# Kernel optimization log

Measured on AMD Instinct MI355X. Metric: run time of the kernel, lower is better.

Reference implementation:

```python
import jax, jax.numpy as jnp
import numpy as np

D_MODEL = 768
D_STATE = 16
D_CONV = 4
EXPAND = 2
HEADDIM = 64
D_INNER = EXPAND * D_MODEL          # 1536
NHEADS = D_INNER // HEADDIM         # 24
CONV_DIM = D_INNER + 2 * D_STATE    # 1568
D_IN_PROJ = 2 * D_INNER + 2 * D_STATE + NHEADS  # 3128
BATCH, SEQ = 4, 2048


def _mamba_params(key, scale=0.02):
    ks = jax.random.split(key, 5)
    return dict(
        in_w=jax.random.normal(ks[0], (D_MODEL, D_IN_PROJ), jnp.float32) * scale,
        conv_w=jax.random.normal(ks[1], (CONV_DIM, D_CONV), jnp.float32) * scale,
        conv_b=jnp.zeros((CONV_DIM,), jnp.float32),
        dt_bias=jax.random.normal(ks[2], (NHEADS,), jnp.float32) * 0.1,
        A_log=jnp.log(jax.random.uniform(ks[3], (NHEADS,), jnp.float32, 1.0, 16.0)),
        D=jnp.ones((NHEADS,), jnp.float32),
        norm_w=jnp.ones((D_INNER,), jnp.float32),
        out_w=jax.random.normal(ks[4], (D_INNER, D_MODEL), jnp.float32) * scale,
    )


def setup_inputs() -> dict:
    key = jax.random.key(0)
    kx, kf, kb, k1, k2 = jax.random.split(key, 5)
    f = _mamba_params(kf)
    b = _mamba_params(kb)
    k1a, k1b = jax.random.split(k1)
    inp = {
        'x': jax.random.normal(kx, (BATCH, SEQ, D_MODEL), jnp.float32),
        'ln1_w': jnp.ones((D_MODEL,), jnp.float32), 'ln1_b': jnp.zeros((D_MODEL,), jnp.float32),
        'ln2_w': jnp.ones((D_MODEL,), jnp.float32), 'ln2_b': jnp.zeros((D_MODEL,), jnp.float32),
        'ffn_w1': jax.random.normal(k1a, (2 * D_MODEL, 4 * D_MODEL), jnp.float32) * 0.02,
        'ffn_b1': jnp.zeros((4 * D_MODEL,), jnp.float32),
        'ffn_w2': jax.random.normal(k1b, (4 * D_MODEL, D_MODEL), jnp.float32) * 0.02,
        'ffn_b2': jnp.zeros((D_MODEL,), jnp.float32),
    }
    for name, p in (('f', f), ('b', b)):
        for k, v in p.items():
            inp[name + '_' + k] = v
    return inp


def _layernorm(x, w, b, eps=1e-5):
    m = jnp.mean(x, -1, keepdims=True)
    v = jnp.mean((x - m) ** 2, -1, keepdims=True)
    return (x - m) * jax.lax.rsqrt(v + eps) * w + b


def _mamba2(u, in_w, conv_w, conv_b, dt_bias, A_log, D, norm_w, out_w):
    b, l, _ = u.shape
    zxbcdt = u @ in_w                               # (b,l,d_in_proj)
    z = zxbcdt[..., :D_INNER]
    xBC = zxbcdt[..., D_INNER:D_INNER + CONV_DIM]
    dt = jax.nn.softplus(zxbcdt[..., -NHEADS:] + dt_bias)   # (b,l,h)
    # depthwise causal conv1d (kernel D_CONV) + SiLU
    xpad = jnp.pad(xBC, ((0, 0), (D_CONV - 1, 0), (0, 0)))
    xc = sum(conv_w[:, k] * xpad[:, k:k + l, :] for k in range(D_CONV)) + conv_b
    xc = jax.nn.silu(xc)
    xh = xc[..., :D_INNER].reshape(b, l, NHEADS, HEADDIM)
    Bm = xc[..., D_INNER:D_INNER + D_STATE]          # (b,l,n), ngroups=1
    Cm = xc[..., D_INNER + D_STATE:]                 # (b,l,n)
    A = -jnp.exp(A_log)                              # (h,)
    dA = jnp.exp(dt * A)                             # (b,l,h)

    def step(h, inp):
        dA_t, dt_t, B_t, C_t, x_t = inp              # (b,h),(b,h),(b,n),(b,n),(b,h,p)
        h = h * dA_t[:, :, None, None] + (dt_t[:, :, None] * x_t)[..., None] * B_t[:, None, None, :]
        y = jnp.einsum('bhpn,bn->bhp', h, C_t)
        return h, y

    h0 = jnp.zeros((b, NHEADS, HEADDIM, D_STATE), u.dtype)
    xs = (dA.transpose(1, 0, 2), dt.transpose(1, 0, 2), Bm.transpose(1, 0, 2),
          Cm.transpose(1, 0, 2), xh.transpose(1, 0, 2, 3))
    _, ys = jax.lax.scan(step, h0, xs)               # ys: (l,b,h,p)
    y = ys.transpose(1, 0, 2, 3) + D[None, None, :, None] * xh
    y = y.reshape(b, l, D_INNER)
    # gated RMSNorm: rmsnorm(y * silu(z)) * weight
    yz = y * jax.nn.silu(z)
    yz = yz * jax.lax.rsqrt(jnp.mean(yz * yz, -1, keepdims=True) + 1e-5) * norm_w
    return yz @ out_w


def reference(x, ln1_w, ln1_b, ln2_w, ln2_b,
              f_in_w, f_conv_w, f_conv_b, f_dt_bias, f_A_log, f_D, f_norm_w, f_out_w,
              b_in_w, b_conv_w, b_conv_b, b_dt_bias, b_A_log, b_D, b_norm_w, b_out_w,
              ffn_w1, ffn_b1, ffn_w2, ffn_b2):
    xn = _layernorm(x, ln1_w, ln1_b)
    fo = _mamba2(xn, f_in_w, f_conv_w, f_conv_b, f_dt_bias, f_A_log, f_D, f_norm_w, f_out_w)
    bo = _mamba2(jnp.flip(xn, 1), b_in_w, b_conv_w, b_conv_b, b_dt_bias, b_A_log, b_D, b_norm_w, b_out_w)
    bo = jnp.flip(bo, 1)
    bi = jnp.concatenate([fo, bo], -1)
    h = jax.nn.gelu(bi @ ffn_w1 + ffn_b1, approximate=False)
    h = jax.nn.gelu(h @ ffn_w2 + ffn_b2, approximate=False)
    # dropout is identity in eval mode
    return _layernorm(x + h, ln2_w, ln2_b)
```

## Files before the change

### kernel.cpp

```cpp
#include <hip/hip_runtime.h>
#include <math.h>

#define BATCH   4
#define SEQ     2048
#define DMODEL  768
#define DSTATE  16
#define DCONV   4
#define HEADDIM 64
#define DINNER  1536
#define NHEADS  24
#define CONVDIM 1568
#define DINPROJ 3128
#define DFFN    3072
#define ROWS    (BATCH*SEQ)
#define QCH     128
#define NCHUNK  (SEQ/QCH)

typedef __attribute__((ext_vector_type(8))) short bhalf8;
typedef __attribute__((ext_vector_type(4))) float floatx4;

__device__ __forceinline__ float gelu_f(float x) {
    return 0.5f * x * (1.0f + erff(x * 0.70710678118654752f));
}

__device__ __forceinline__ void splitT(float v, unsigned short& h, unsigned short& l) {
    unsigned u = __float_as_uint(v);
    h = (unsigned short)(u >> 16);
    float rem = v - __uint_as_float(u & 0xFFFF0000u);
    l = (unsigned short)(__float_as_uint(rem) >> 16);
}

__device__ __forceinline__ float2 blockReduce2(float a, float b) {
    #pragma unroll
    for (int o = 32; o > 0; o >>= 1) {
        a += __shfl_down(a, o, 64);
        b += __shfl_down(b, o, 64);
    }
    __shared__ float sa[4], sb[4];
    int w = threadIdx.x >> 6, lane = threadIdx.x & 63;
    if (lane == 0) { sa[w] = a; sb[w] = b; }
    __syncthreads();
    if (threadIdx.x == 0) {
        int nw = blockDim.x >> 6;
        for (int i = 1; i < nw; ++i) { a += sa[i]; b += sb[i]; }
        sa[0] = a; sb[0] = b;
    }
    __syncthreads();
    return make_float2(sa[0], sb[0]);
}

__global__ __launch_bounds__(256) void ln_kernel(
    const float* __restrict__ x, const float* __restrict__ res,
    const float* __restrict__ w, const float* __restrict__ b,
    float* __restrict__ out)
{
    int r = blockIdx.x;
    const float* xr = x + (size_t)r * DMODEL;
    float v[3]; float s = 0.f, ss = 0.f;
    #pragma unroll
    for (int i = 0; i < 3; ++i) {
        int c = threadIdx.x + i * 256;
        float t = xr[c];
        if (res) t += res[(size_t)r * DMODEL + c];
        v[i] = t; s += t; ss += t * t;
    }
    float2 red = blockReduce2(s, ss);
    float mean = red.x * (1.0f / DMODEL);
    float var  = red.y * (1.0f / DMODEL) - mean * mean;
    float inv  = rsqrtf(var + 1e-5f);
    #pragma unroll
    for (int i = 0; i < 3; ++i) {
        int c = threadIdx.x + i * 256;
        out[(size_t)r * DMODEL + c] = (v[i] - mean) * inv * w[c] + b[c];
    }
}

__global__ __launch_bounds__(256) void wconv(
    const float* __restrict__ W, unsigned short* __restrict__ TH,
    unsigned short* __restrict__ TL, int K, int N)
{
    __shared__ float t[32][33];
    int tx = threadIdx.x & 31, ty = threadIdx.x >> 5;
    int kb = blockIdx.y * 32, nb = blockIdx.x * 32;
    #pragma unroll
    for (int i = 0; i < 4; ++i) {
        int k = kb + ty + i * 8, n = nb + tx;
        t[ty + i * 8][tx] = (k < K && n < N) ? W[(size_t)k * N + n] : 0.f;
    }
    __syncthreads();
    #pragma unroll
    for (int i = 0; i < 4; ++i) {
        int n = nb + ty + i * 8, k = kb + tx;
        if (n < N && k < K) {
            float v = t[tx][ty + i * 8];
            unsigned u = __float_as_uint(v);
            unsigned rr = u + 0x7FFFu + ((u >> 16) & 1u);
            unsigned short hi = (unsigned short)(rr >> 16);
            float rem = v - __uint_as_float(((unsigned)hi) << 16);
            unsigned u2 = __float_as_uint(rem);
            unsigned r2 = u2 + 0x7FFFu + ((u2 >> 16) & 1u);
            unsigned short lo = (unsigned short)(r2 >> 16);
            TH[(size_t)n * K + k] = hi;
            TL[(size_t)n * K + k] = lo;
        }
    }
}

__global__ __launch_bounds__(256) void gemm3(
    const float* __restrict__ Ag,
    const unsigned short* __restrict__ BHg, const unsigned short* __restrict__ BLg,
    float* __restrict__ C, const float* __restrict__ bias,
    int M, int N, int K, int lda, int ldc, int coloff,
    int revA, int revC, int act)
{
    __shared__ unsigned short AsH[128 * 40], AsL[128 * 40];
    __shared__ unsigned short BsH[128 * 40], BsL[128 * 40];

    const int tid = threadIdx.x;
    const int m0 = blockIdx.y * 128;
    const int n0 = blockIdx.x * 128;

    const int r  = tid >> 1;
    const int sg = (tid & 1) * 16;
    int arow = m0 + r;
    if (revA) arow = (arow & ~(SEQ - 1)) + (SEQ - 1 - (arow & (SEQ - 1)));
    const size_t abase = (size_t)arow * lda;
    const int brow = n0 + r;
    const bool bok = brow < N;
    const size_t bbase = (size_t)brow * K;

    float4 fa[4];
    bhalf8 rb0, rb1, rb2, rb3;
    const bhalf8 bz = {0, 0, 0, 0, 0, 0, 0, 0};

    auto gload = [&](int k0) {
        size_t ao = abase + k0 + sg;
        #pragma unroll
        for (int q = 0; q < 4; ++q) fa[q] = *(const float4*)(Ag + ao + 4 * q);
        if (bok) {
            size_t bo = bbase + k0 + sg;
            rb0 = *(const bhalf8*)(BHg + bo);
            rb1 = *(const bhalf8*)(BHg + bo + 8);
            rb2 = *(const bhalf8*)(BLg + bo);
            rb3 = *(const bhalf8*)(BLg + bo + 8);
        } else { rb0 = bz; rb1 = bz; rb2 = bz; rb3 = bz; }
    };

    auto stage = [&]() {
        const float* fs = (const float*)fa;
        bhalf8 h0, h1, l0, l1;
        #pragma unroll
        for (int e = 0; e < 8; ++e) {
            unsigned short h, l;
            splitT(fs[e], h, l);     h0[e] = (short)h; l0[e] = (short)l;
            splitT(fs[8 + e], h, l); h1[e] = (short)h; l1[e] = (short)l;
        }
        *(bhalf8*)&AsH[r * 40 + sg]     = h0;
        *(bhalf8*)&AsH[r * 40 + sg + 8] = h1;
        *(bhalf8*)&AsL[r * 40 + sg]     = l0;
        *(bhalf8*)&AsL[r * 40 + sg + 8] = l1;
        *(bhalf8*)&BsH[r * 40 + sg]     = rb0;
        *(bhalf8*)&BsH[r * 40 + sg + 8] = rb1;
        *(bhalf8*)&BsL[r * 40 + sg]     = rb2;
        *(bhalf8*)&BsL[r * 40 + sg + 8] = rb3;
    };

    const int w = tid >> 6, lane = tid & 63;
    const int rw = (w >> 1) * 64, cw = (w & 1) * 64;
    const int lr = lane & 15;
    const int lq = lane >> 4;

    floatx4 acc[4][4];
    const floatx4 fz = {0.f, 0.f, 0.f, 0.f};
    #pragma unroll
    for (int i = 0; i < 4; ++i)
        #pragma unroll
        for (int j = 0; j < 4; ++j) acc[i][j] = fz;

    const int ktiles = K >> 5;
    gload(0);
    for (int kt = 0; kt < ktiles; ++kt) {
        __syncthreads();
        stage();
        __syncthreads();
        if (kt + 1 < ktiles) gload((kt + 1) * 32);

        bhalf8 ah[4], al[4], bh[4], bl[4];
        #pragma unroll
        for (int i = 0; i < 4; ++i) {
            ah[i] = *(const bhalf8*)&AsH[(rw + i * 16 + lr) * 40 + lq * 8];
            al[i] = *(const bhalf8*)&AsL[(rw + i * 16 + lr) * 40 + lq * 8];
            bh[i] = *(const bhalf8*)&BsH[(cw + i * 16 + lr) * 40 + lq * 8];
            bl[i] = *(const bhalf8*)&BsL[(cw + i * 16 + lr) * 40 + lq * 8];
        }
        #pragma unroll
        for (int i = 0; i < 4; ++i)
            #pragma unroll
            for (int j = 0; j < 4; ++j) {
                acc[i][j] = __builtin_amdgcn_mfma_f32_16x16x32_bf16(ah[i], bh[j], acc[i][j], 0, 0, 0);
                acc[i][j] = __builtin_amdgcn_mfma_f32_16x16x32_bf16(ah[i], bl[j], acc[i][j], 0, 0, 0);
                acc[i][j] = __builtin_amdgcn_mfma_f32_16x16x32_bf16(al[i], bh[j], acc[i][j], 0, 0, 0);
            }
    }

    #pragma unroll
    for (int i = 0; i < 4; ++i) {
        #pragma unroll
        for (int j = 0; j < 4; ++j) {
            int gc = n0 + cw + j * 16 + lr;
            if (gc < N) {
                float bv = bias ? bias[gc] : 0.f;
                #pragma unroll
                for (int rg = 0; rg < 4; ++rg) {
                    int gm = m0 + rw + i * 16 + lq * 4 + rg;
                    if (revC) gm = (gm & ~(SEQ - 1)) + (SEQ - 1 - (gm & (SEQ - 1)));
                    float v = acc[i][j][rg] + bv;
                    if (act) v = gelu_f(v);
                    C[(size_t)gm * ldc + coloff + gc] = v;
                }
            }
        }
    }
}

__global__ __launch_bounds__(256) void conv_kernel(
    const float* __restrict__ zx, const float* __restrict__ cw,
    const float* __restrict__ cb, float* __restrict__ xcv,
    float* __restrict__ bc)
{
    int c = blockIdx.x * 256 + threadIdx.x;
    int r = blockIdx.y;
    if (c >= CONVDIM) return;
    int t = r & (SEQ - 1);
    int rb = r & ~(SEQ - 1);
    float acc = cb[c];
    #pragma unroll
    for (int k = 0; k < DCONV; ++k) {
        int tt = t - (DCONV - 1) + k;
        if (tt >= 0)
            acc += cw[c * DCONV + k] * zx[(size_t)(rb + tt) * DINPROJ + DINNER + c];
    }
    float v = acc / (1.0f + expf(-acc));
    if (c < DINNER) xcv[(size_t)r * DINNER + c] = v;
    else            bc[(size_t)r * 32 + (c - DINNER)] = v;
}

__global__ __launch_bounds__(256) void dt_kernel(
    const float* __restrict__ zx, const float* __restrict__ dt_bias,
    const float* __restrict__ A_log, float* __restrict__ dtda)
{
    int i = blockIdx.x * 256 + threadIdx.x;
    if (i >= ROWS * NHEADS) return;
    int r = i / NHEADS, h = i - r * NHEADS;
    float v = zx[(size_t)r * DINPROJ + (DINPROJ - NHEADS) + h] + dt_bias[h];
    float dt = (v > 20.f) ? v : log1pf(expf(v));
    float A = -expf(A_log[h]);
    dtda[(size_t)r * 48 + h] = dt;
    dtda[(size_t)r * 48 + 24 + h] = expf(dt * A);
}

__global__ __launch_bounds__(64) void scan_a(
    const float* __restrict__ xcv, const float* __restrict__ bc,
    const float* __restrict__ dtda, const float* __restrict__ Dp,
    float* __restrict__ yout, float* __restrict__ S, float* __restrict__ cd)
{
    int blk = blockIdx.x;
    int bh = blk / NCHUNK, c = blk - bh * NCHUNK;
    int b = bh / NHEADS, h = bh - b * NHEADS;
    int p = threadIdx.x;
    float hs[DSTATE] = {};
    float Dv = Dp[h];
    float cum = 1.f;
    int t0 = c * QCH;
    for (int t = t0; t < t0 + QCH; ++t) {
        size_t r = (size_t)b * SEQ + t;
        float dt = dtda[r * 48 + h];
        float dA = dtda[r * 48 + 24 + h];
        float x  = xcv[r * DINNER + h * HEADDIM + p];
        cum *= dA;
        float coef = dt * x;
        const float* bcr = bc + r * 32;
        float y = 0.f;
        #pragma unroll
        for (int n = 0; n < DSTATE; ++n) {
            hs[n] = hs[n] * dA + coef * bcr[n];
            y += hs[n] * bcr[16 + n];
        }
        yout[r * DINPROJ + DINNER + h * HEADDIM + p] = y + Dv * x;
        if (p == 0) cd[r * NHEADS + h] = cum;
    }
    float* Sp = S + (((size_t)bh * NCHUNK + c) * HEADDIM + p) * DSTATE;
    #pragma unroll
    for (int n = 0; n < DSTATE; ++n) Sp[n] = hs[n];
}

__global__ __launch_bounds__(64) void scan_b(
    const float* __restrict__ cd, float* __restrict__ S)
{
    int bh = blockIdx.x;
    int b = bh / NHEADS, h = bh - b * NHEADS;
    int p = threadIdx.x;
    float H[DSTATE] = {};
    for (int c = 0; c < NCHUNK; ++c) {
        float* Sp = S + (((size_t)bh * NCHUNK + c) * HEADDIM + p) * DSTATE;
        float P = cd[((size_t)b * SEQ + c * QCH + QCH - 1) * NHEADS + h];
        float s[DSTATE];
        #pragma unroll
        for (int n = 0; n < DSTATE; ++n) s[n] = Sp[n];
        #pragma unroll
        for (int n = 0; n < DSTATE; ++n) Sp[n] = H[n];
        #pragma unroll
        for (int n = 0; n < DSTATE; ++n) H[n] = P * H[n] + s[n];
    }
}

__global__ __launch_bounds__(64) void scan_c(
    const float* __restrict__ bc, const float* __restrict__ cd,
    const float* __restrict__ S, float* __restrict__ yout)
{
    int blk = blockIdx.x;
    int bh = blk / (NCHUNK - 1), c = blk - bh * (NCHUNK - 1) + 1;
    int b = bh / NHEADS, h = bh - b * NHEADS;
    int p = threadIdx.x;
    const float* Hp = S + (((size_t)bh * NCHUNK + c) * HEADDIM + p) * DSTATE;
    float H[DSTATE];
    #pragma unroll
    for (int n = 0; n < DSTATE; ++n) H[n] = Hp[n];
    int t0 = c * QCH;
    for (int t = t0; t < t0 + QCH; ++t) {
        size_t r = (size_t)b * SEQ + t;
        const float* Cr = bc + r * 32 + 16;
        float dot = 0.f;
        #pragma unroll
        for (int n = 0; n < DSTATE; ++n) dot += H[n] * Cr[n];
        float cum = cd[r * NHEADS + h];
        yout[r * DINPROJ + DINNER + h * HEADDIM + p] += cum * dot;
    }
}

__global__ __launch_bounds__(256) void gnorm_kernel(
    const float* __restrict__ zx, const float* __restrict__ nw,
    float* __restrict__ out)
{
    int r = blockIdx.x;
    const float* zr = zx + (size_t)r * DINPROJ;
    float v[6]; float ss = 0.f;
    #pragma unroll
    for (int i = 0; i < 6; ++i) {
        int c = threadIdx.x + i * 256;
        float z = zr[c];
        float y = zr[DINNER + c];
        float t = y * z / (1.0f + expf(-z));
        v[i] = t; ss += t * t;
    }
    float2 red = blockReduce2(ss, 0.f);
    float sc = rsqrtf(red.x * (1.0f / DINNER) + 1e-5f);
    #pragma unroll
    for (int i = 0; i < 6; ++i) {
        int c = threadIdx.x + i * 256;
        out[(size_t)r * DINNER + c] = v[i] * sc * nw[c];
    }
}

extern "C" void kernel_launch(void* const* d_in, const int* in_sizes, int n_in,
                              void* d_out, int out_size, void* d_ws, size_t ws_size,
                              hipStream_t stream)
{
    (void)in_sizes; (void)n_in; (void)out_size; (void)ws_size;
    const float* x     = (const float*)d_in[0];
    const float* ln1w  = (const float*)d_in[1];
    const float* ln1b  = (const float*)d_in[2];
    const float* ln2w  = (const float*)d_in[3];
    const float* ln2b  = (const float*)d_in[4];
    const float* ffnw1 = (const float*)d_in[5];
    const float* ffnb1 = (const float*)d_in[6];
    const float* ffnw2 = (const float*)d_in[7];
    const float* ffnb2 = (const float*)d_in[8];
    const float* p[2][8];
    for (int d = 0; d < 2; ++d)
        for (int i = 0; i < 8; ++i)
            p[d][i] = (const float*)d_in[9 + d * 8 + i];

    float* ws   = (float*)d_ws;
    float* zx   = ws;
    float* bi   = zx + (size_t)ROWS * DINPROJ;
    float* S    = bi + (size_t)ROWS * DINNER;
    float* Wbuf = S  + (size_t)ROWS * DINNER;
    float* bcb  = Wbuf + 2402304;
    float* dtda = bcb + (size_t)ROWS * 32;
    float* Sbuf = Wbuf;
    float* cdbf = Wbuf + (size_t)BATCH * NHEADS * NCHUNK * HEADDIM * DSTATE;
    float* xn   = (float*)d_out;
    float* xcv  = S;
    float* zn   = S;
    float* hmid = zx;
    float* ffo  = S + 4718592;

    ln_kernel<<<ROWS, 256, 0, stream>>>(x, nullptr, ln1w, ln1b, xn);

    for (int d = 0; d < 2; ++d) {
        unsigned short* WH = (unsigned short*)Wbuf;
        unsigned short* WL = WH + (size_t)DINPROJ * DMODEL;
        wconv<<<dim3((DINPROJ + 31) / 32, DMODEL / 32), 256, 0, stream>>>(
            p[d][0], WH, WL, DMODEL, DINPROJ);
        gemm3<<<dim3((DINPROJ + 127) / 128, ROWS / 128), 256, 0, stream>>>(
            xn, WH, WL, zx, nullptr,
            ROWS, DINPROJ, DMODEL, DMODEL, DINPROJ, 0, d, 0, 0);
        conv_kernel<<<dim3(7, ROWS), 256, 0, stream>>>(zx, p[d][1], p[d][2], xcv, bcb);
        dt_kernel<<<(ROWS * NHEADS + 255) / 256, 256, 0, stream>>>(
            zx, p[d][3], p[d][4], dtda);
        scan_a<<<BATCH * NHEADS * NCHUNK, 64, 0, stream>>>(
            xcv, bcb, dtda, p[d][5], zx, Sbuf, cdbf);
        scan_b<<<BATCH * NHEADS, 64, 0, stream>>>(cdbf, Sbuf);
        scan_c<<<BATCH * NHEADS * (NCHUNK - 1), 64, 0, stream>>>(
            bcb, cdbf, Sbuf, zx);
        gnorm_kernel<<<ROWS, 256, 0, stream>>>(zx, p[d][6], zn);
        unsigned short* WL2 = WH + (size_t)DMODEL * DINNER;
        wconv<<<dim3(DMODEL / 32, DINNER / 32), 256, 0, stream>>>(
            p[d][7], WH, WL2, DINNER, DMODEL);
        gemm3<<<dim3(DMODEL / 128, ROWS / 128), 256, 0, stream>>>(
            zn, WH, WL2, bi, nullptr,
            ROWS, DMODEL, DINNER, DINNER, DINNER, d * DMODEL, 0, d, 0);
    }

    {
        unsigned short* WH = (unsigned short*)S;
        unsigned short* WL = WH + (size_t)DFFN * DINNER;
        wconv<<<dim3(DFFN / 32, DINNER / 32), 256, 0, stream>>>(
            ffnw1, WH, WL, DINNER, DFFN);
        gemm3<<<dim3(DFFN / 128, ROWS / 128), 256, 0, stream>>>(
            bi, WH, WL, hmid, ffnb1,
            ROWS, DFFN, DINNER, DINNER, DFFN, 0, 0, 0, 1);
    }
    {
        unsigned short* WH = (unsigned short*)S;
        unsigned short* WL = WH + (size_t)DMODEL * DFFN;
        wconv<<<dim3(DMODEL / 32, DFFN / 32), 256, 0, stream>>>(
            ffnw2, WH, WL, DFFN, DMODEL);
        gemm3<<<dim3(DMODEL / 128, ROWS / 128), 256, 0, stream>>>(
            hmid, WH, WL, ffo, ffnb2,
            ROWS, DMODEL, DFFN, DFFN, DMODEL, 0, 0, 0, 1);
    }
    ln_kernel<<<ROWS, 256, 0, stream>>>(x, ffo, ln2w, ln2b, (float*)d_out);
}
```

Baseline: 1.564 ms.

## Pre-split GEMM activations into bf16 hi/lo and load tiles directly into LDS

Producer kernels (layernorm, gated norm, and the GEMM epilogues that feed later GEMMs) now write their outputs already split into bf16 high/low halves with round-to-nearest. This removes the per-tile fp32-to-bf16 split that each GEMM block used to redo in its inner loop. The GEMM fills its shared-memory tiles with global_load_lds, skipping the register staging step, and uses an XOR-swizzled unpadded layout to avoid bank conflicts. The trade-off is a single LDS buffer: the next tile's loads start only after the fragments have been read into registers, which may reduce overlap of loads with MFMA work. The split rounding also differs slightly from the old truncation.

```diff
diff --git a/kernel.cpp b/kernel.cpp
--- a/kernel.cpp
+++ b/kernel.cpp
@@ -23,11 +23,21 @@
     return 0.5f * x * (1.0f + erff(x * 0.70710678118654752f));
 }
 
-__device__ __forceinline__ void splitT(float v, unsigned short& h, unsigned short& l) {
+__device__ __forceinline__ void splitRNE(float v, unsigned short& h, unsigned short& l) {
     unsigned u = __float_as_uint(v);
-    h = (unsigned short)(u >> 16);
-    float rem = v - __uint_as_float(u & 0xFFFF0000u);
-    l = (unsigned short)(__float_as_uint(rem) >> 16);
+    unsigned rr = u + 0x7FFFu + ((u >> 16) & 1u);
+    unsigned short hi = (unsigned short)(rr >> 16);
+    float rem = v - __uint_as_float(((unsigned)hi) << 16);
+    unsigned u2 = __float_as_uint(rem);
+    unsigned r2 = u2 + 0x7FFFu + ((u2 >> 16) & 1u);
+    h = hi;
+    l = (unsigned short)(r2 >> 16);
+}
+
+__device__ __forceinline__ void gl16(const unsigned short* g, unsigned short* l) {
+    __builtin_amdgcn_global_load_lds(
+        (const __attribute__((address_space(1))) void*)g,
+        (__attribute__((address_space(3))) void*)l, 16, 0, 0);
 }
 
 __device__ __forceinline__ float2 blockReduce2(float a, float b) {
@@ -75,6 +85,35 @@
     }
 }
 
+__global__ __launch_bounds__(256) void ln_split_kernel(
+    const float* __restrict__ x,
+    const float* __restrict__ w, const float* __restrict__ b,
+    unsigned short* __restrict__ H, unsigned short* __restrict__ L)
+{
+    int r = blockIdx.x;
+    const float* xr = x + (size_t)r * DMODEL;
+    float v[3]; float s = 0.f, ss = 0.f;
+    #pragma unroll
+    for (int i = 0; i < 3; ++i) {
+        int c = threadIdx.x + i * 256;
+        float t = xr[c];
+        v[i] = t; s += t; ss += t * t;
+    }
+    float2 red = blockReduce2(s, ss);
+    float mean = red.x * (1.0f / DMODEL);
+    float var  = red.y * (1.0f / DMODEL) - mean * mean;
+    float inv  = rsqrtf(var + 1e-5f);
+    #pragma unroll
+    for (int i = 0; i < 3; ++i) {
+        int c = threadIdx.x + i * 256;
+        float o = (v[i] - mean) * inv * w[c] + b[c];
+        unsigned short h, l;
+        splitRNE(o, h, l);
+        H[(size_t)r * DMODEL + c] = h;
+        L[(size_t)r * DMODEL + c] = l;
+    }
+}
+
 __global__ __launch_bounds__(256) void wconv(
     const float* __restrict__ W, unsigned short* __restrict__ TH,
     unsigned short* __restrict__ TL, int K, int N)
@@ -92,14 +131,8 @@
     for (int i = 0; i < 4; ++i) {
         int n = nb + ty + i * 8, k = kb + tx;
         if (n < N && k < K) {
-            float v = t[tx][ty + i * 8];
-            unsigned u = __float_as_uint(v);
-            unsigned rr = u + 0x7FFFu + ((u >> 16) & 1u);
-            unsigned short hi = (unsigned short)(rr >> 16);
-            float rem = v - __uint_as_float(((unsigned)hi) << 16);
-            unsigned u2 = __float_as_uint(rem);
-            unsigned r2 = u2 + 0x7FFFu + ((u2 >> 16) & 1u);
-            unsigned short lo = (unsigned short)(r2 >> 16);
+            unsigned short hi, lo;
+            splitRNE(t[tx][ty + i * 8], hi, lo);
             TH[(size_t)n * K + k] = hi;
             TL[(size_t)n * K + k] = lo;
         }
@@ -107,62 +140,47 @@
 }
 
 __global__ __launch_bounds__(256) void gemm3(
-    const float* __restrict__ Ag,
+    const unsigned short* __restrict__ AHg, const unsigned short* __restrict__ ALg,
     const unsigned short* __restrict__ BHg, const unsigned short* __restrict__ BLg,
-    float* __restrict__ C, const float* __restrict__ bias,
-    int M, int N, int K, int lda, int ldc, int coloff,
+    float* __restrict__ C, unsigned short* __restrict__ CHo, unsigned short* __restrict__ CLo,
+    const float* __restrict__ bias,
+    int M, int N, int K, int ldc, int coloff,
     int revA, int revC, int act)
 {
-    __shared__ unsigned short AsH[128 * 40], AsL[128 * 40];
-    __shared__ unsigned short BsH[128 * 40], BsL[128 * 40];
+    (void)M;
+    __shared__ __align__(16) unsigned short AsH[128 * 32], AsL[128 * 32];
+    __shared__ __align__(16) unsigned short BsH[128 * 32], BsL[128 * 32];
 
     const int tid = threadIdx.x;
     const int m0 = blockIdx.y * 128;
     const int n0 = blockIdx.x * 128;
 
-    const int r  = tid >> 1;
-    const int sg = (tid & 1) * 16;
-    int arow = m0 + r;
-    if (revA) arow = (arow & ~(SEQ - 1)) + (SEQ - 1 - (arow & (SEQ - 1)));
-    const size_t abase = (size_t)arow * lda;
-    const int brow = n0 + r;
-    const bool bok = brow < N;
-    const size_t bbase = (size_t)brow * K;
-
-    float4 fa[4];
-    bhalf8 rb0, rb1, rb2, rb3;
-    const bhalf8 bz = {0, 0, 0, 0, 0, 0, 0, 0};
-
-    auto gload = [&](int k0) {
-        size_t ao = abase + k0 + sg;
-        #pragma unroll
-        for (int q = 0; q < 4; ++q) fa[q] = *(const float4*)(Ag + ao + 4 * q);
-        if (bok) {
-            size_t bo = bbase + k0 + sg;
-            rb0 = *(const bhalf8*)(BHg + bo);
-            rb1 = *(const bhalf8*)(BHg + bo + 8);
-            rb2 = *(const bhalf8*)(BLg + bo);
-            rb3 = *(const bhalf8*)(BLg + bo + 8);
-        } else { rb0 = bz; rb1 = bz; rb2 = bz; rb3 = bz; }
+    size_t aoff[2], boff[2];
+    int lofs[2];
+    #pragma unroll
+    for (int q = 0; q < 2; ++q) {
+        int row = (tid >> 2) + 64 * q;
+        int sd  = (tid & 3) ^ ((row >> 1) & 3);
+        int ar = m0 + row;
+        if (revA) ar = (ar & ~(SEQ - 1)) + (SEQ - 1 - (ar & (SEQ - 1)));
+        aoff[q] = (size_t)ar * K + sd * 8;
+        boff[q] = (size_t)(n0 + row) * K + sd * 8;
+        lofs[q] = (tid + 256 * q) * 8;
+    }
+
+    auto stage = [&](int k0) {
+        #pragma unroll
+        for (int q = 0; q < 2; ++q) {
+            gl16(AHg + aoff[q] + k0, AsH + lofs[q]);
+            gl16(ALg + aoff[q] + k0, AsL + lofs[q]);
+            gl16(BHg + boff[q] + k0, BsH + lofs[q]);
+            gl16(BLg + boff[q] + k0, BsL + lofs[q]);
+        }
     };
 
-    auto stage = [&]() {
-        const float* fs = (const float*)fa;
-        bhalf8 h0, h1, l0, l1;
-        #pragma unroll
-        for (int e = 0; e < 8; ++e) {
-            unsigned short h, l;
-            splitT(fs[e], h, l);     h0[e] = (short)h; l0[e] = (short)l;
-            splitT(fs[8 + e], h, l); h1[e] = (short)h; l1[e] = (short)l;
-        }
-        *(bhalf8*)&AsH[r * 40 + sg]     = h0;
-        *(bhalf8*)&AsH[r * 40 + sg + 8] = h1;
-        *(bhalf8*)&AsL[r * 40 + sg]     = l0;
-        *(bhalf8*)&AsL[r * 40 + sg + 8] = l1;
-        *(bhalf8*)&BsH[r * 40 + sg]     = rb0;
-        *(bhalf8*)&BsH[r * 40 + sg + 8] = rb1;
-        *(bhalf8*)&BsL[r * 40 + sg]     = rb2;
-        *(bhalf8*)&BsL[r * 40 + sg + 8] = rb3;
+    auto frag = [&](const unsigned short* buf, int row, int slot) -> bhalf8 {
+        int sp = slot ^ ((row >> 1) & 3);
+        return *(const bhalf8*)(buf + row * 32 + sp * 8);
     };
 
     const int w = tid >> 6, lane = tid & 63;
@@ -178,21 +196,21 @@
         for (int j = 0; j < 4; ++j) acc[i][j] = fz;
 
     const int ktiles = K >> 5;
-    gload(0);
+    stage(0);
     for (int kt = 0; kt < ktiles; ++kt) {
         __syncthreads();
-        stage();
+        bhalf8 ah[4], al[4], bh[4], bl[4];
+        #pragma unroll
+        for (int i = 0; i < 4; ++i) {
+            int ra = rw + i * 16 + lr;
+            int rb = cw + i * 16 + lr;
+            ah[i] = frag(AsH, ra, lq);
+            al[i] = frag(AsL, ra, lq);
+            bh[i] = frag(BsH, rb, lq);
+            bl[i] = frag(BsL, rb, lq);
+        }
         __syncthreads();
-        if (kt + 1 < ktiles) gload((kt + 1) * 32);
-
-        bhalf8 ah[4], al[4], bh[4], bl[4];
-        #pragma unroll
-        for (int i = 0; i < 4; ++i) {
-            ah[i] = *(const bhalf8*)&AsH[(rw + i * 16 + lr) * 40 + lq * 8];
-            al[i] = *(const bhalf8*)&AsL[(rw + i * 16 + lr) * 40 + lq * 8];
-            bh[i] = *(const bhalf8*)&BsH[(cw + i * 16 + lr) * 40 + lq * 8];
-            bl[i] = *(const bhalf8*)&BsL[(cw + i * 16 + lr) * 40 + lq * 8];
-        }
+        if (kt + 1 < ktiles) stage((kt + 1) * 32);
         #pragma unroll
         for (int i = 0; i < 4; ++i)
             #pragma unroll
@@ -216,7 +234,14 @@
                     if (revC) gm = (gm & ~(SEQ - 1)) + (SEQ - 1 - (gm & (SEQ - 1)));
                     float v = acc[i][j][rg] + bv;
                     if (act) v = gelu_f(v);
-                    C[(size_t)gm * ldc + coloff + gc] = v;
+                    size_t o = (size_t)gm * ldc + coloff + gc;
+                    if (CHo) {
+                        unsigned short h, l;
+                        splitRNE(v, h, l);
+                        CHo[o] = h; CLo[o] = l;
+                    } else {
+                        C[o] = v;
+                    }
                 }
             }
         }
@@ -340,7 +365,7 @@
 
 __global__ __launch_bounds__(256) void gnorm_kernel(
     const float* __restrict__ zx, const float* __restrict__ nw,
-    float* __restrict__ out)
+    unsigned short* __restrict__ H, unsigned short* __restrict__ L)
 {
     int r = blockIdx.x;
     const float* zr = zx + (size_t)r * DINPROJ;
@@ -358,7 +383,11 @@
     #pragma unroll
     for (int i = 0; i < 6; ++i) {
         int c = threadIdx.x + i * 256;
-        out[(size_t)r * DINNER + c] = v[i] * sc * nw[c];
+        float o = v[i] * sc * nw[c];
+        unsigned short h, l;
+        splitRNE(o, h, l);
+        H[(size_t)r * DINNER + c] = h;
+        L[(size_t)r * DINNER + c] = l;
     }
 }
 
@@ -390,13 +419,19 @@
     float* dtda = bcb + (size_t)ROWS * 32;
     float* Sbuf = Wbuf;
     float* cdbf = Wbuf + (size_t)BATCH * NHEADS * NCHUNK * HEADDIM * DSTATE;
-    float* xn   = (float*)d_out;
-    float* xcv  = S;
-    float* zn   = S;
-    float* hmid = zx;
-    float* ffo  = S + 4718592;
-
-    ln_kernel<<<ROWS, 256, 0, stream>>>(x, nullptr, ln1w, ln1b, xn);
+
+    unsigned short* xnH = (unsigned short*)d_out;
+    unsigned short* xnL = xnH + (size_t)ROWS * DMODEL;
+    float* xcv = S;
+    unsigned short* znH = (unsigned short*)S;
+    unsigned short* znL = znH + (size_t)ROWS * DINNER;
+    unsigned short* biH = (unsigned short*)bi;
+    unsigned short* biL = biH + (size_t)ROWS * DINNER;
+    unsigned short* hmH = (unsigned short*)zx;
+    unsigned short* hmL = hmH + (size_t)ROWS * DFFN;
+    float* ffo = S + 4718592;
+
+    ln_split_kernel<<<ROWS, 256, 0, stream>>>(x, ln1w, ln1b, xnH, xnL);
 
     for (int d = 0; d < 2; ++d) {
         unsigned short* WH = (unsigned short*)Wbuf;
@@ -404,8 +439,8 @@
         wconv<<<dim3((DINPROJ + 31) / 32, DMODEL / 32), 256, 0, stream>>>(
             p[d][0], WH, WL, DMODEL, DINPROJ);
         gemm3<<<dim3((DINPROJ + 127) / 128, ROWS / 128), 256, 0, stream>>>(
-            xn, WH, WL, zx, nullptr,
-            ROWS, DINPROJ, DMODEL, DMODEL, DINPROJ, 0, d, 0, 0);
+            xnH, xnL, WH, WL, zx, nullptr, nullptr, nullptr,
+            ROWS, DINPROJ, DMODEL, DINPROJ, 0, d, 0, 0);
         conv_kernel<<<dim3(7, ROWS), 256, 0, stream>>>(zx, p[d][1], p[d][2], xcv, bcb);
         dt_kernel<<<(ROWS * NHEADS + 255) / 256, 256, 0, stream>>>(
             zx, p[d][3], p[d][4], dtda);
@@ -414,13 +449,13 @@
         scan_b<<<BATCH * NHEADS, 64, 0, stream>>>(cdbf, Sbuf);
         scan_c<<<BATCH * NHEADS * (NCHUNK - 1), 64, 0, stream>>>(
             bcb, cdbf, Sbuf, zx);
-        gnorm_kernel<<<ROWS, 256, 0, stream>>>(zx, p[d][6], zn);
+        gnorm_kernel<<<ROWS, 256, 0, stream>>>(zx, p[d][6], znH, znL);
         unsigned short* WL2 = WH + (size_t)DMODEL * DINNER;
         wconv<<<dim3(DMODEL / 32, DINNER / 32), 256, 0, stream>>>(
             p[d][7], WH, WL2, DINNER, DMODEL);
         gemm3<<<dim3(DMODEL / 128, ROWS / 128), 256, 0, stream>>>(
-            zn, WH, WL2, bi, nullptr,
-            ROWS, DMODEL, DINNER, DINNER, DINNER, d * DMODEL, 0, d, 0);
+            znH, znL, WH, WL2, nullptr, biH, biL, nullptr,
+            ROWS, DMODEL, DINNER, DINNER, d * DMODEL, 0, d, 0);
     }
 
     {
@@ -429,8 +464,8 @@
         wconv<<<dim3(DFFN / 32, DINNER / 32), 256, 0, stream>>>(
             ffnw1, WH, WL, DINNER, DFFN);
         gemm3<<<dim3(DFFN / 128, ROWS / 128), 256, 0, stream>>>(
-            bi, WH, WL, hmid, ffnb1,
-            ROWS, DFFN, DINNER, DINNER, DFFN, 0, 0, 0, 1);
+            biH, biL, WH, WL, nullptr, hmH, hmL, ffnb1,
+            ROWS, DFFN, DINNER, DFFN, 0, 0, 0, 1);
     }
     {
         unsigned short* WH = (unsigned short*)S;
@@ -438,8 +473,8 @@
         wconv<<<dim3(DMODEL / 32, DFFN / 32), 256, 0, stream>>>(
             ffnw2, WH, WL, DFFN, DMODEL);
         gemm3<<<dim3(DMODEL / 128, ROWS / 128), 256, 0, stream>>>(
-            hmid, WH, WL, ffo, ffnb2,
-            ROWS, DMODEL, DFFN, DFFN, DMODEL, 0, 0, 0, 1);
+            hmH, hmL, WH, WL, ffo, nullptr, nullptr, ffnb2,
+            ROWS, DMODEL, DFFN, DMODEL, 0, 0, 0, 1);
     }
     ln_kernel<<<ROWS, 256, 0, stream>>>(x, ffo, ln2w, ln2b, (float*)d_out);
 }
```

Result: faster. 1.461 ms (-6.6%).
